# Kernel optimization log

Hardware: AMD Instinct MI355X
Metric: run time of the kernel (lower is better)

The kernel has to match this reference:

```python
import jax, jax.numpy as jnp
import numpy as np

B, H, W, DIM, R = 8, 64, 64, 768, 16
_DN = ('NHWC', 'HWIO', 'NHWC')


def _conv(x, k):
    # stride-1 SAME conv == torch Conv2d(padding=k//2) for 3x3 and 1x1 kernels
    return jax.lax.conv_general_dilated(x, k, (1, 1), 'SAME', dimension_numbers=_DN)


def setup_inputs() -> dict:
    key = jax.random.key(0)
    ks = jax.random.split(key, 16)
    s = 0.02
    return {
        'x': jax.random.normal(ks[0], (B, H, W, DIM), jnp.float32),
        'W_qkv': jax.random.normal(ks[1], (DIM, 3 * DIM), jnp.float32) * s,
        'b_qkv': jax.random.normal(ks[2], (3 * DIM,), jnp.float32) * s,
        'Wa_q': jax.random.normal(ks[3], (DIM, R), jnp.float32) * s,
        'Wb_q': jax.random.normal(ks[4], (R, DIM), jnp.float32) * s,
        'Wa_v': jax.random.normal(ks[5], (DIM, R), jnp.float32) * s,
        'Wb_v': jax.random.normal(ks[6], (R, DIM), jnp.float32) * s,
        'K_q3': jax.random.normal(ks[7], (3, 3, R, R), jnp.float32) * s,
        'b_q3': jax.random.normal(ks[8], (R,), jnp.float32) * s,
        'K_v3': jax.random.normal(ks[9], (3, 3, R, R), jnp.float32) * s,
        'b_v3': jax.random.normal(ks[10], (R,), jnp.float32) * s,
        'K_q1': jax.random.normal(ks[11], (1, 1, R, R), jnp.float32) * s,
        'b_q1': jax.random.normal(ks[12], (R,), jnp.float32) * s,
        'K_v1': jax.random.normal(ks[13], (1, 1, R, R), jnp.float32) * s,
        'b_v1': jax.random.normal(ks[14], (R,), jnp.float32) * s,
    }


def reference(x, W_qkv, b_qkv, Wa_q, Wb_q, Wa_v, Wb_v,
              K_q3, b_q3, K_v3, b_v3, K_q1, b_q1, K_v1, b_v1):
    dim = x.shape[-1]
    # base QKV projection: [B,H,W,3*dim]
    qkv = jnp.einsum('bhwc,cd->bhwd', x, W_qkv) + b_qkv
    # low-rank down-projections: [B,H,W,r]
    a_q = x @ Wa_q
    a_v = x @ Wa_v
    # NHWC convs replace the permute->conv->permute dance in the torch code
    mid_q = _conv(a_q, K_q3) + b_q3 + _conv(a_q, K_q1) + b_q1 + a_q
    mid_v = _conv(a_v, K_v3) + b_v3 + _conv(a_v, K_v1) + b_v1 + a_v
    new_q = mid_q @ Wb_q  # [B,H,W,dim]
    new_v = mid_v @ Wb_v
    qkv = qkv.at[..., :dim].add(new_q)
    qkv = qkv.at[..., -dim:].add(new_v)
    return qkv
```

## Files before the change

### kernel.cpp

```cpp
#include <hip/hip_runtime.h>

typedef __bf16 bf16;
typedef __attribute__((ext_vector_type(8))) __bf16 bf16x8;
typedef __attribute__((ext_vector_type(4))) float f32x4;

#define AS1U(p) ((const __attribute__((address_space(1))) unsigned int*)(p))
#define AS3U(p) ((__attribute__((address_space(3))) unsigned int*)(p))

__device__ __forceinline__ unsigned short f2bf(float f) {
    union { float f; unsigned int u; } a; a.f = f;
    unsigned int u = a.u;
    u += 0x7fffu + ((u >> 16) & 1u);
    return (unsigned short)(u >> 16);
}
__device__ __forceinline__ unsigned int pk2(float a, float b) {
    return (unsigned int)f2bf(a) | ((unsigned int)f2bf(b) << 16);
}

#define MTOT 32768
#define DIM  768
#define KP   832
#define NOUT 2304

__global__ __launch_bounds__(256) void bbuild_kernel(
    const float* __restrict__ Wqkv, const float* __restrict__ Wbq,
    const float* __restrict__ Wbv, const float* __restrict__ Waq,
    const float* __restrict__ Wav, unsigned short* __restrict__ Bt,
    unsigned short* __restrict__ WaT)
{
    const int bx = blockIdx.x;
    const int t = threadIdx.x;
    if (bx < 432) {
        __shared__ float Ts[64][65];
        const int kt = bx % 12, nt = bx / 12;
        #pragma unroll
        for (int it = 0; it < 4; ++it) {
            int idx = it * 256 + t;
            int kr = idx >> 4;
            int nc = (idx & 15) * 4;
            float4 v = *(const float4*)(Wqkv + (size_t)(kt * 64 + kr) * NOUT + nt * 64 + nc);
            Ts[kr][nc + 0] = v.x; Ts[kr][nc + 1] = v.y;
            Ts[kr][nc + 2] = v.z; Ts[kr][nc + 3] = v.w;
        }
        __syncthreads();
        #pragma unroll
        for (int it = 0; it < 4; ++it) {
            int idx = it * 256 + t;
            int nr = idx >> 4;
            int kc = (idx & 15) * 4;
            ushort4 u;
            u.x = f2bf(Ts[kc + 0][nr]); u.y = f2bf(Ts[kc + 1][nr]);
            u.z = f2bf(Ts[kc + 2][nr]); u.w = f2bf(Ts[kc + 3][nr]);
            *(ushort4*)(Bt + (size_t)(nt * 64 + nr) * KP + kt * 64 + kc) = u;
        }
    } else if (bx < 576) {
        int idx = (bx - 432) * 256 + t;
        int n = idx >> 4;
        int k = 768 + (idx & 15) * 4;
        ushort4 u;
        unsigned short* up = (unsigned short*)&u;
        #pragma unroll
        for (int j = 0; j < 4; ++j) {
            int kk = k + j;
            float v = 0.f;
            if (kk < 784) { if (n < 768) v = Wbq[(size_t)(kk - 768) * 768 + n]; }
            else if (kk < 800) { if (n >= 1536) v = Wbv[(size_t)(kk - 784) * 768 + (n - 1536)]; }
            up[j] = f2bf(v);
        }
        *(ushort4*)(Bt + (size_t)n * KP + k) = u;
    } else {
        int idx = (bx - 576) * 256 + t;
        int n = idx / 768, k = idx % 768;
        float v = (n < 16) ? Waq[(size_t)k * 16 + n] : Wav[(size_t)k * 16 + (n - 16)];
        WaT[(size_t)n * 768 + k] = f2bf(v);
    }
}

__global__ __launch_bounds__(256) void prep_kernel(
    const float* __restrict__ x, const bf16* __restrict__ WaT,
    unsigned short* __restrict__ Ap, float* __restrict__ aq, float* __restrict__ av)
{
    __shared__ bf16 Xs[64 * 64];
    const int t = threadIdx.x;
    const int wave = t >> 6, lane = t & 63;
    const int l15 = lane & 15, q = lane >> 4;
    const int p0 = blockIdx.x * 64;
    const int row = t >> 2, c16 = (t & 3) * 16;
    const int r8 = row & 7, ch0 = c16 >> 3;
    f32x4 acc[2] = {};

    for (int kt = 0; kt < 12; ++kt) {
        const float* xp = x + (size_t)(p0 + row) * DIM + kt * 64 + c16;
        float4 v0 = *(const float4*)(xp + 0);
        float4 v1 = *(const float4*)(xp + 4);
        float4 v2 = *(const float4*)(xp + 8);
        float4 v3 = *(const float4*)(xp + 12);
        uint4 u0, u1;
        u0.x = pk2(v0.x, v0.y); u0.y = pk2(v0.z, v0.w);
        u0.z = pk2(v1.x, v1.y); u0.w = pk2(v1.z, v1.w);
        u1.x = pk2(v2.x, v2.y); u1.y = pk2(v2.z, v2.w);
        u1.z = pk2(v3.x, v3.y); u1.w = pk2(v3.z, v3.w);
        unsigned short* apq = Ap + (size_t)(p0 + row) * KP + kt * 64 + c16;
        *(uint4*)(apq) = u0;
        *(uint4*)(apq + 8) = u1;
        __syncthreads();
        *(uint4*)(Xs + row * 64 + ((ch0 + 0) ^ r8) * 8) = u0;
        *(uint4*)(Xs + row * 64 + ((ch0 + 1) ^ r8) * 8) = u1;
        __syncthreads();
        bf16x8 bfr[2][2];
        #pragma unroll
        for (int kk = 0; kk < 2; ++kk)
            #pragma unroll
            for (int nf = 0; nf < 2; ++nf)
                bfr[kk][nf] = *(const bf16x8*)(WaT + (size_t)(nf * 16 + l15) * 768
                                               + kt * 64 + kk * 32 + q * 8);
        #pragma unroll
        for (int kk = 0; kk < 2; ++kk) {
            int phys = ((kk << 2) + q) ^ (l15 & 7);
            bf16x8 af = *(const bf16x8*)(Xs + (wave * 16 + l15) * 64 + phys * 8);
            acc[0] = __builtin_amdgcn_mfma_f32_16x16x32_bf16(af, bfr[kk][0], acc[0], 0, 0, 0);
            acc[1] = __builtin_amdgcn_mfma_f32_16x16x32_bf16(af, bfr[kk][1], acc[1], 0, 0, 0);
        }
    }
    const int m = wave * 16 + q * 4;
    #pragma unroll
    for (int r = 0; r < 4; ++r) {
        aq[(size_t)(p0 + m + r) * 16 + l15] = acc[0][r];
        av[(size_t)(p0 + m + r) * 16 + l15] = acc[1][r];
    }
    uint4 z; z.x = z.y = z.z = z.w = 0u;
    *(uint4*)(Ap + (size_t)(p0 + row) * KP + 800 + (t & 3) * 8) = z;
}

__global__ __launch_bounds__(256) void conv_mid_kernel(
    const float* __restrict__ aq, const float* __restrict__ av,
    const float* __restrict__ Kq3, const float* __restrict__ bq3,
    const float* __restrict__ Kv3, const float* __restrict__ bv3,
    const float* __restrict__ Kq1, const float* __restrict__ bq1,
    const float* __restrict__ Kv1, const float* __restrict__ bv1,
    unsigned short* __restrict__ Ap)
{
    const int bx = blockIdx.x;
    const int qv   = bx & 1;
    const int tile = (bx >> 1) & 15;
    const int b    = bx >> 5;
    const float* a  = qv ? av  : aq;
    const float* K3 = qv ? Kv3 : Kq3;
    const float* K1 = qv ? Kv1 : Kq1;
    const float* b3 = qv ? bv3 : bq3;
    const float* b1 = qv ? bv1 : bq1;

    __shared__ float K3s[9][16][16];
    __shared__ float K1s[16][16];
    const int t = threadIdx.x;
    for (int i = t; i < 9 * 256; i += 256) ((float*)K3s)[i] = K3[i];
    ((float*)K1s)[t] = K1[t];
    __syncthreads();

    const int lh = t >> 4, lw = t & 15;
    const int h = (tile >> 2) * 16 + lh;
    const int w = (tile & 3) * 16 + lw;

    float acc[16];
    const float* ac = a + (((size_t)b * 64 + h) * 64 + w) * 16;
    float cen[16];
    #pragma unroll
    for (int i4 = 0; i4 < 4; ++i4) {
        float4 qd = ((const float4*)ac)[i4];
        cen[i4 * 4 + 0] = qd.x; cen[i4 * 4 + 1] = qd.y;
        cen[i4 * 4 + 2] = qd.z; cen[i4 * 4 + 3] = qd.w;
    }
    #pragma unroll
    for (int o = 0; o < 16; ++o) acc[o] = b3[o] + b1[o] + cen[o];
    #pragma unroll
    for (int i = 0; i < 16; ++i) {
        float vi = cen[i];
        #pragma unroll
        for (int o = 0; o < 16; ++o) acc[o] += vi * K1s[i][o];
    }
    for (int dh = -1; dh <= 1; ++dh) {
        for (int dw = -1; dw <= 1; ++dw) {
            int hh = h + dh, ww = w + dw;
            if ((unsigned)hh < 64u && (unsigned)ww < 64u) {
                const float* ap = a + (((size_t)b * 64 + hh) * 64 + ww) * 16;
                float v[16];
                #pragma unroll
                for (int i4 = 0; i4 < 4; ++i4) {
                    float4 qd = ((const float4*)ap)[i4];
                    v[i4 * 4 + 0] = qd.x; v[i4 * 4 + 1] = qd.y;
                    v[i4 * 4 + 2] = qd.z; v[i4 * 4 + 3] = qd.w;
                }
                const int tap = (dh + 1) * 3 + (dw + 1);
                #pragma unroll
                for (int i = 0; i < 16; ++i) {
                    float vi = v[i];
                    #pragma unroll
                    for (int o = 0; o < 16; ++o) acc[o] += vi * K3s[tap][i][o];
                }
            }
        }
    }
    unsigned short* dst = Ap + (((size_t)b * 64 + h) * 64 + w) * KP + 768 + qv * 16;
    #pragma unroll
    for (int o4 = 0; o4 < 4; ++o4) {
        ushort4 u;
        u.x = f2bf(acc[o4 * 4 + 0]); u.y = f2bf(acc[o4 * 4 + 1]);
        u.z = f2bf(acc[o4 * 4 + 2]); u.w = f2bf(acc[o4 * 4 + 3]);
        *(ushort4*)(dst + o4 * 4) = u;
    }
}

__global__ __launch_bounds__(512, 2) void gemm_kernel(
    const bf16* __restrict__ A, const bf16* __restrict__ Bt,
    const float* __restrict__ bias, float* __restrict__ out)
{
    __shared__ bf16 As[2][256 * 64];
    __shared__ bf16 Bs[2][256 * 64];
    const int t = threadIdx.x;
    const int wave = t >> 6, lane = t & 63;
    const int wm = wave >> 2, wn = wave & 3;
    const int m0 = blockIdx.y * 256, n0 = blockIdx.x * 256;

    const int sr8 = lane >> 3;
    const int slc = (lane & 7) ^ sr8;
    const bf16* gA = A  + (size_t)(m0 + wave * 8 + sr8) * KP + slc * 8;
    const bf16* gB = Bt + (size_t)(n0 + wave * 8 + sr8) * KP + slc * 8;
    const int ldsbase = wave * 512 + lane * 8;

    const int l15 = lane & 15;
    const int q   = lane >> 4;
    const int l7  = lane & 7;

    f32x4 acc[8][4] = {};

    auto STAGE = [&](int kt1, int bufi) {
        const int k0 = kt1 * 64;
        #pragma unroll
        for (int it = 0; it < 4; ++it) {
            __builtin_amdgcn_global_load_lds(AS1U(gA + (size_t)(it * 64) * KP + k0),
                AS3U(&As[bufi][it * 4096 + ldsbase]), 16, 0, 0);
            __builtin_amdgcn_global_load_lds(AS1U(gB + (size_t)(it * 64) * KP + k0),
                AS3U(&Bs[bufi][it * 4096 + ldsbase]), 16, 0, 0);
        }
    };

    STAGE(0, 0);

    for (int kt = 0; kt < 13; ++kt) {
        const int cur = kt & 1;
        __builtin_amdgcn_sched_barrier(0);
        if (kt < 12) {
            STAGE(kt + 1, cur ^ 1);
            asm volatile("s_waitcnt vmcnt(8)" ::: "memory");
        } else {
            asm volatile("s_waitcnt vmcnt(0)" ::: "memory");
        }
        __builtin_amdgcn_s_barrier();

        const bf16* as = &As[cur][0];
        const bf16* bs = &Bs[cur][0];

        bf16x8 bfr[2][4];
        #pragma unroll
        for (int kk = 0; kk < 2; ++kk) {
            const int phys = ((kk << 2) + q) ^ l7;
            #pragma unroll
            for (int ni = 0; ni < 4; ++ni)
                bfr[kk][ni] = *(const bf16x8*)(bs + (wn * 64 + ni * 16 + l15) * 64 + phys * 8);
        }

        #pragma unroll
        for (int p = 0; p < 4; ++p) {
            bf16x8 af[2][2];
            #pragma unroll
            for (int j = 0; j < 2; ++j) {
                const int mi = p * 2 + j;
                #pragma unroll
                for (int kk = 0; kk < 2; ++kk) {
                    const int phys = ((kk << 2) + q) ^ l7;
                    af[j][kk] = *(const bf16x8*)(as + (wm * 128 + mi * 16 + l15) * 64 + phys * 8);
                }
            }
            __builtin_amdgcn_s_barrier();
            asm volatile("s_waitcnt lgkmcnt(0)" ::: "memory");
            __builtin_amdgcn_s_setprio(1);
            #pragma unroll
            for (int j = 0; j < 2; ++j)
                #pragma unroll
                for (int ni = 0; ni < 4; ++ni)
                    #pragma unroll
                    for (int kk = 0; kk < 2; ++kk)
                        acc[p * 2 + j][ni] = __builtin_amdgcn_mfma_f32_16x16x32_bf16(
                            af[j][kk], bfr[kk][ni], acc[p * 2 + j][ni], 0, 0, 0);
            __builtin_amdgcn_s_setprio(0);
            __builtin_amdgcn_s_barrier();
        }
    }

    #pragma unroll
    for (int ni = 0; ni < 4; ++ni) {
        const int col = n0 + wn * 64 + ni * 16 + l15;
        const float bv = bias[col];
        #pragma unroll
        for (int mi = 0; mi < 8; ++mi) {
            const int rbase = m0 + wm * 128 + mi * 16 + (q << 2);
            #pragma unroll
            for (int r = 0; r < 4; ++r)
                out[(size_t)(rbase + r) * NOUT + col] = acc[mi][ni][r] + bv;
        }
    }
}

extern "C" void kernel_launch(void* const* d_in, const int* in_sizes, int n_in,
                              void* d_out, int out_size, void* d_ws, size_t ws_size,
                              hipStream_t stream) {
    const float* x    = (const float*)d_in[0];
    const float* Wqkv = (const float*)d_in[1];
    const float* bqkv = (const float*)d_in[2];
    const float* Waq  = (const float*)d_in[3];
    const float* Wbq  = (const float*)d_in[4];
    const float* Wav  = (const float*)d_in[5];
    const float* Wbv  = (const float*)d_in[6];
    const float* Kq3  = (const float*)d_in[7];
    const float* bq3  = (const float*)d_in[8];
    const float* Kv3  = (const float*)d_in[9];
    const float* bv3  = (const float*)d_in[10];
    const float* Kq1  = (const float*)d_in[11];
    const float* bq1  = (const float*)d_in[12];
    const float* Kv1  = (const float*)d_in[13];
    const float* bv1  = (const float*)d_in[14];
    float* out = (float*)d_out;

    char* ws = (char*)d_ws;
    unsigned short* Ap  = (unsigned short*)ws;
    float* aq           = (float*)(ws + 54525952);
    float* av           = (float*)(ws + 54525952 + 2097152);
    unsigned short* Bt  = (unsigned short*)(ws + 54525952 + 4194304);
    unsigned short* WaT = (unsigned short*)(ws + 62554112);

    bbuild_kernel<<<672, 256, 0, stream>>>(Wqkv, Wbq, Wbv, Waq, Wav, Bt, WaT);
    prep_kernel<<<MTOT / 64, 256, 0, stream>>>(x, (const bf16*)WaT, Ap, aq, av);
    conv_mid_kernel<<<256, 256, 0, stream>>>(aq, av, Kq3, bq3, Kv3, bv3,
                                             Kq1, bq1, Kv1, bv1, Ap);
    gemm_kernel<<<dim3(NOUT / 256, MTOT / 256), 512, 0, stream>>>(
        (const bf16*)Ap, (const bf16*)Bt, bqkv, out);
}
```

Measured before the change: 601.9 us.

## Load GEMM B fragments directly from global into registers, drop B LDS staging

The GEMM stops staging the weight tile in shared memory. Each wave now loads its B fragments (128 columns by 64 k) straight from global memory into registers, while only the A tile is double-buffered in LDS, and the wave layout changes to 4x2 with each wave holding 64x128. The launch becomes a 1D grid remapped so consecutive blocks sharing M rows land on the same XCD, and launch bounds are raised to target more occupancy. This is meant to halve LDS traffic and LDS footprint and to improve L2 reuse, at the cost of redundant global reads of B across waves and more VGPRs per wave.

```diff
diff --git a/kernel.cpp b/kernel.cpp
--- a/kernel.cpp
+++ b/kernel.cpp
@@ -210,100 +210,86 @@
     }
 }
 
-__global__ __launch_bounds__(512, 2) void gemm_kernel(
+__global__ __launch_bounds__(512, 4) void gemm_kernel(
     const bf16* __restrict__ A, const bf16* __restrict__ Bt,
     const float* __restrict__ bias, float* __restrict__ out)
 {
     __shared__ bf16 As[2][256 * 64];
-    __shared__ bf16 Bs[2][256 * 64];
     const int t = threadIdx.x;
     const int wave = t >> 6, lane = t & 63;
-    const int wm = wave >> 2, wn = wave & 3;
-    const int m0 = blockIdx.y * 256, n0 = blockIdx.x * 256;
+    const int wm = wave & 3, wn = wave >> 2;
+
+    const int bid = blockIdx.x;
+    const int xcd = bid & 7, w = bid >> 3;
+    const int mb = xcd * 16 + w / 9, nb = w % 9;
+    const int m0 = mb * 256, n0 = nb * 256;
 
     const int sr8 = lane >> 3;
     const int slc = (lane & 7) ^ sr8;
-    const bf16* gA = A  + (size_t)(m0 + wave * 8 + sr8) * KP + slc * 8;
-    const bf16* gB = Bt + (size_t)(n0 + wave * 8 + sr8) * KP + slc * 8;
+    const bf16* gA = A + (size_t)(m0 + wave * 8 + sr8) * KP + slc * 8;
     const int ldsbase = wave * 512 + lane * 8;
 
-    const int l15 = lane & 15;
-    const int q   = lane >> 4;
-    const int l7  = lane & 7;
-
-    f32x4 acc[8][4] = {};
+    const int l15 = lane & 15, q = lane >> 4, l7 = lane & 7;
+
+    f32x4 acc[4][8] = {};
 
     auto STAGE = [&](int kt1, int bufi) {
         const int k0 = kt1 * 64;
         #pragma unroll
-        for (int it = 0; it < 4; ++it) {
+        for (int it = 0; it < 4; ++it)
             __builtin_amdgcn_global_load_lds(AS1U(gA + (size_t)(it * 64) * KP + k0),
                 AS3U(&As[bufi][it * 4096 + ldsbase]), 16, 0, 0);
-            __builtin_amdgcn_global_load_lds(AS1U(gB + (size_t)(it * 64) * KP + k0),
-                AS3U(&Bs[bufi][it * 4096 + ldsbase]), 16, 0, 0);
-        }
     };
+
+    const bf16* gBw = Bt + (size_t)(n0 + wn * 128 + l15) * KP + q * 8;
 
     STAGE(0, 0);
 
     for (int kt = 0; kt < 13; ++kt) {
         const int cur = kt & 1;
-        __builtin_amdgcn_sched_barrier(0);
+        bf16x8 bfr[2][8];
+        #pragma unroll
+        for (int ni = 0; ni < 8; ++ni)
+            #pragma unroll
+            for (int kk = 0; kk < 2; ++kk)
+                bfr[kk][ni] = *(const bf16x8*)(gBw + (size_t)(ni * 16) * KP
+                                               + kt * 64 + kk * 32);
         if (kt < 12) {
             STAGE(kt + 1, cur ^ 1);
-            asm volatile("s_waitcnt vmcnt(8)" ::: "memory");
+            asm volatile("s_waitcnt vmcnt(20)\n\ts_barrier" ::: "memory");
         } else {
-            asm volatile("s_waitcnt vmcnt(0)" ::: "memory");
-        }
-        __builtin_amdgcn_s_barrier();
+            asm volatile("s_waitcnt vmcnt(16)\n\ts_barrier" ::: "memory");
+        }
 
         const bf16* as = &As[cur][0];
-        const bf16* bs = &Bs[cur][0];
-
-        bf16x8 bfr[2][4];
-        #pragma unroll
-        for (int kk = 0; kk < 2; ++kk) {
-            const int phys = ((kk << 2) + q) ^ l7;
-            #pragma unroll
-            for (int ni = 0; ni < 4; ++ni)
-                bfr[kk][ni] = *(const bf16x8*)(bs + (wn * 64 + ni * 16 + l15) * 64 + phys * 8);
-        }
-
         #pragma unroll
         for (int p = 0; p < 4; ++p) {
-            bf16x8 af[2][2];
-            #pragma unroll
-            for (int j = 0; j < 2; ++j) {
-                const int mi = p * 2 + j;
+            bf16x8 af[2];
+            #pragma unroll
+            for (int kk = 0; kk < 2; ++kk) {
+                const int phys = ((kk << 2) + q) ^ l7;
+                af[kk] = *(const bf16x8*)(as + (wm * 64 + p * 16 + l15) * 64 + phys * 8);
+            }
+            __builtin_amdgcn_s_setprio(1);
+            #pragma unroll
+            for (int ni = 0; ni < 8; ++ni)
                 #pragma unroll
-                for (int kk = 0; kk < 2; ++kk) {
-                    const int phys = ((kk << 2) + q) ^ l7;
-                    af[j][kk] = *(const bf16x8*)(as + (wm * 128 + mi * 16 + l15) * 64 + phys * 8);
-                }
-            }
-            __builtin_amdgcn_s_barrier();
-            asm volatile("s_waitcnt lgkmcnt(0)" ::: "memory");
-            __builtin_amdgcn_s_setprio(1);
-            #pragma unroll
-            for (int j = 0; j < 2; ++j)
-                #pragma unroll
-                for (int ni = 0; ni < 4; ++ni)
-                    #pragma unroll
-                    for (int kk = 0; kk < 2; ++kk)
-                        acc[p * 2 + j][ni] = __builtin_amdgcn_mfma_f32_16x16x32_bf16(
-                            af[j][kk], bfr[kk][ni], acc[p * 2 + j][ni], 0, 0, 0);
+                for (int kk = 0; kk < 2; ++kk)
+                    acc[p][ni] = __builtin_amdgcn_mfma_f32_16x16x32_bf16(
+                        af[kk], bfr[kk][ni], acc[p][ni], 0, 0, 0);
             __builtin_amdgcn_s_setprio(0);
-            __builtin_amdgcn_s_barrier();
-        }
-    }
-
-    #pragma unroll
-    for (int ni = 0; ni < 4; ++ni) {
-        const int col = n0 + wn * 64 + ni * 16 + l15;
+            if (p < 3) __builtin_amdgcn_s_barrier();
+        }
+        asm volatile("s_barrier" ::: "memory");
+    }
+
+    #pragma unroll
+    for (int ni = 0; ni < 8; ++ni) {
+        const int col = n0 + wn * 128 + ni * 16 + l15;
         const float bv = bias[col];
         #pragma unroll
-        for (int mi = 0; mi < 8; ++mi) {
-            const int rbase = m0 + wm * 128 + mi * 16 + (q << 2);
+        for (int mi = 0; mi < 4; ++mi) {
+            const int rbase = m0 + wm * 64 + mi * 16 + (q << 2);
             #pragma unroll
             for (int r = 0; r < 4; ++r)
                 out[(size_t)(rbase + r) * NOUT + col] = acc[mi][ni][r] + bv;
@@ -342,6 +328,6 @@
     prep_kernel<<<MTOT / 64, 256, 0, stream>>>(x, (const bf16*)WaT, Ap, aq, av);
     conv_mid_kernel<<<256, 256, 0, stream>>>(aq, av, Kq3, bq3, Kv3, bv3,
                                              Kq1, bq1, Kv1, bv1, Ap);
-    gemm_kernel<<<dim3(NOUT / 256, MTOT / 256), 512, 0, stream>>>(
+    gemm_kernel<<<1152, 512, 0, stream>>>(
         (const bf16*)Ap, (const bf16*)Bt, bqkv, out);
 }
```

After: 1.526 ms. 154% more time.
